# Performance work log

Measured on AMD Instinct MI355X. Metric: run time of the kernel, lower is better.

Reference implementation:

```python
import jax, jax.numpy as jnp
import numpy as np

N_NODES = 50000
N_EDGES = 800000
F_IN = 256
F_OUT = 64
HEADS = 4
LEAKY_ALPHA = 0.2


def setup_inputs() -> dict:
    key = jax.random.key(0)
    ks = jax.random.split(key, 8)
    x = jax.random.normal(ks[0], (N_NODES, F_IN), dtype=jnp.float32)
    W = jax.random.normal(ks[1], (HEADS, F_IN, F_OUT), dtype=jnp.float32) * 0.05
    a_self = jax.random.normal(ks[2], (HEADS, F_OUT), dtype=jnp.float32) * 0.05
    a_neigh = jax.random.normal(ks[3], (HEADS, F_OUT), dtype=jnp.float32) * 0.05
    bias = jnp.zeros((HEADS, F_OUT), dtype=jnp.float32)
    adj_val = jnp.ones((N_EDGES,), dtype=jnp.float32)
    edge_row = jax.random.randint(ks[4], (N_EDGES,), 0, N_NODES, dtype=jnp.int32)
    edge_col = jax.random.randint(ks[5], (N_EDGES,), 0, N_NODES, dtype=jnp.int32)
    return {"x": x, "W": W, "a_self": a_self, "a_neigh": a_neigh,
            "bias": bias, "adj_val": adj_val,
            "edge_row": edge_row, "edge_col": edge_col}


def reference(x, W, a_self, a_neigh, bias, adj_val, edge_row, edge_col):
    N = x.shape[0]
    # per-head projected features: [H, N, F_out]
    feats = jnp.einsum('nf,hfo->hno', x, W)
    # attention logits per node: [H, N]
    s_self = jnp.einsum('hno,ho->hn', feats, a_self)
    s_neigh = jnp.einsum('hno,ho->hn', feats, a_neigh)
    # edge scores at sparse adjacency positions: [H, E]
    z = s_self[:, edge_row] + s_neigh[:, edge_col]
    e = jnp.where(z > 0, z, LEAKY_ALPHA * z) * adj_val[None, :]

    def seg_softmax(e_h):
        # sparse softmax over each row's nonzero entries
        m = jax.ops.segment_max(e_h, edge_row, num_segments=N)
        ex = jnp.exp(e_h - m[edge_row])
        s = jax.ops.segment_sum(ex, edge_row, num_segments=N)
        return ex / s[edge_row]

    alpha = jax.vmap(seg_softmax)(e)  # [H, E]

    def aggregate(alpha_h, feat_h):
        # sparse-dense matmul: out[i] = sum_{j in N(i)} alpha_ij * feat[j]
        return jax.ops.segment_sum(alpha_h[:, None] * feat_h[edge_col],
                                   edge_row, num_segments=N)

    out = jax.vmap(aggregate)(alpha, feats) + bias[:, None, :]  # [H, N, F_out]
    # concat heads -> [N, H*F_out], then activation
    out = jnp.transpose(out, (1, 0, 2)).reshape(N, -1)
    return jax.nn.relu(out)
```

## Files before the change

kernel.cpp:

```cpp
#include <hip/hip_runtime.h>
#include <hip/hip_fp16.h>
#include <math.h>

#define NN 50000
#define NE 800000
#define FIN 256
#define FOUT 64
#define HEADS 4
#define HF 256
#define CAP 64

typedef unsigned short u16;
typedef unsigned int u32;
typedef __attribute__((ext_vector_type(4))) u16 u16x4;
typedef __attribute__((ext_vector_type(8))) u16 u16x8;
typedef __attribute__((ext_vector_type(8))) short short8;
typedef __attribute__((ext_vector_type(4))) float f32x4;

__device__ __forceinline__ u16 f2bf(float x) {
  u32 u = __float_as_uint(x);
  u += 0x7fffu + ((u >> 16) & 1u);
  return (u16)(u >> 16);
}
__device__ __forceinline__ float bf2f(u16 u) {
  return __uint_as_float(((u32)u) << 16);
}
__device__ __forceinline__ void gload_lds16(u16* lds, const u16* g) {
  __builtin_amdgcn_global_load_lds(
      (const __attribute__((address_space(1))) u32*)g,
      (__attribute__((address_space(3))) u32*)lds, 16, 0, 0);
}

#define BT_B   256
#define ZERO_B 196
__global__ __launch_bounds__(256) void tiny_pre_k(const float* __restrict__ W,
                                                  u16* __restrict__ Bt,
                                                  int* __restrict__ cnt) {
  const int b = blockIdx.x, tid = threadIdx.x;
  if (b < BT_B) {
    int t = b * 256 + tid;
    int ho = t >> 8, f = t & 255;
    int h = ho >> 6, o = ho & 63;
    Bt[t] = f2bf(W[h * (FIN * FOUT) + f * FOUT + o]);
  } else {
    int i = (b - BT_B) * 256 + tid;
    if (i < NN) cnt[i] = 0;
  }
}

__global__ __launch_bounds__(512) void gemm_lg_k(const float* __restrict__ X,
                                                 const u16* __restrict__ Bt,
                                                 u16* __restrict__ C,
                                                 const float* __restrict__ a_self,
                                                 const float* __restrict__ a_neigh,
                                                 float* __restrict__ sself,
                                                 float* __restrict__ sneigh,
                                                 int M) {
  __shared__ __align__(16) u16 smA[128 * 64];
  __shared__ __align__(16) u16 smB[256 * 64];
  const int tid = threadIdx.x;
  const int m0 = blockIdx.x * 128;
  const int lane = tid & 63, wid = tid >> 6;
  const int wr = wid >> 2, wc = wid & 3;
  const int arow = tid >> 3;
  const int acol = (tid & 7) * 8;
  f32x4 acc[4][4] = {};

  for (int k0 = 0; k0 < FIN; k0 += 64) {
    float4 p[2][2];
#pragma unroll
    for (int c = 0; c < 2; ++c) {
      int row = m0 + c * 64 + arow;
      if (row > M - 1) row = M - 1;
      const float* ap = X + (size_t)row * 256 + k0 + acol;
      p[c][0] = *(const float4*)ap;
      p[c][1] = *(const float4*)(ap + 4);
    }
#pragma unroll
    for (int c = 0; c < 4; ++c) {
      int row = c * 64 + arow;
      gload_lds16(&smB[(c * 64 + arow) * 64 + acol], Bt + row * 256 + k0 + acol);
    }
#pragma unroll
    for (int c = 0; c < 2; ++c) {
      u16x8 av = { f2bf(p[c][0].x), f2bf(p[c][0].y), f2bf(p[c][0].z), f2bf(p[c][0].w),
                   f2bf(p[c][1].x), f2bf(p[c][1].y), f2bf(p[c][1].z), f2bf(p[c][1].w) };
      *(u16x8*)&smA[(c * 64 + arow) * 64 + acol] = av;
    }
    asm volatile("s_waitcnt vmcnt(0)" ::: "memory");
    __syncthreads();
#pragma unroll
    for (int kk = 0; kk < 2; ++kk) {
      const int kb = kk * 32 + (lane >> 4) * 8;
      short8 aF[4], bF[4];
#pragma unroll
      for (int mi = 0; mi < 4; ++mi)
        aF[mi] = *(const short8*)&smA[(wr * 64 + mi * 16 + (lane & 15)) * 64 + kb];
#pragma unroll
      for (int ni = 0; ni < 4; ++ni)
        bF[ni] = *(const short8*)&smB[(wc * 64 + ni * 16 + (lane & 15)) * 64 + kb];
#pragma unroll
      for (int mi = 0; mi < 4; ++mi)
#pragma unroll
        for (int ni = 0; ni < 4; ++ni)
          acc[mi][ni] = __builtin_amdgcn_mfma_f32_16x16x32_bf16(aF[mi], bF[ni], acc[mi][ni], 0, 0, 0);
    }
    __syncthreads();
  }
#pragma unroll
  for (int mi = 0; mi < 4; ++mi) {
#pragma unroll
    for (int ni = 0; ni < 4; ++ni) {
      f32x4 a = acc[mi][ni];
      int col = wc * 64 + ni * 16 + (lane & 15);
#pragma unroll
      for (int r = 0; r < 4; ++r) {
        int row = m0 + wr * 64 + mi * 16 + (lane >> 4) * 4 + r;
        if (row < M) C[(size_t)row * 256 + col] = f2bf(a[r]);
      }
    }
  }
  float asv[4], anv[4];
#pragma unroll
  for (int ni = 0; ni < 4; ++ni) {
    int col = wc * 64 + ni * 16 + (lane & 15);
    asv[ni] = a_self[col];
    anv[ni] = a_neigh[col];
  }
#pragma unroll
  for (int mi = 0; mi < 4; ++mi) {
#pragma unroll
    for (int r = 0; r < 4; ++r) {
      float ds = 0.f, dn = 0.f;
#pragma unroll
      for (int ni = 0; ni < 4; ++ni) {
        float v = acc[mi][ni][r];
        ds = fmaf(v, asv[ni], ds);
        dn = fmaf(v, anv[ni], dn);
      }
#pragma unroll
      for (int off = 1; off < 16; off <<= 1) {
        ds += __shfl_xor(ds, off, 64);
        dn += __shfl_xor(dn, off, 64);
      }
      if ((lane & 15) == 0) {
        int row = m0 + wr * 64 + mi * 16 + (lane >> 4) * 4 + r;
        if (row < M) {
          sself[row * 4 + wc] = ds;
          sneigh[row * 4 + wc] = dn;
        }
      }
    }
  }
}

__global__ __launch_bounds__(256) void scatter_wk(const int* __restrict__ erow,
                                                  const int* __restrict__ ecol,
                                                  const float* __restrict__ adj,
                                                  const float4* __restrict__ sself4,
                                                  const float4* __restrict__ sneigh4,
                                                  int* __restrict__ cnt,
                                                  u16* __restrict__ scol,
                                                  u16x4* __restrict__ swt) {
  int e = blockIdx.x * 256 + threadIdx.x;
  int r = erow[e];
  int c = ecol[e];
  float av = adj[e];
  float4 ss = sself4[r];
  float4 nb = sneigh4[c];
  float z0 = ss.x + nb.x, z1 = ss.y + nb.y, z2 = ss.z + nb.z, z3 = ss.w + nb.w;
  float w0 = __expf((z0 > 0.f ? z0 : 0.2f * z0) * av);
  float w1 = __expf((z1 > 0.f ? z1 : 0.2f * z1) * av);
  float w2 = __expf((z2 > 0.f ? z2 : 0.2f * z2) * av);
  float w3 = __expf((z3 > 0.f ? z3 : 0.2f * z3) * av);
  __half2 h01 = __floats2half2_rn(w0, w1);
  __half2 h23 = __floats2half2_rn(w2, w3);
  u32 u01 = *(u32*)&h01, u23 = *(u32*)&h23;
  int p = atomicAdd(&cnt[r], 1);
  if (p < CAP) {
    int slot = r * CAP + p;
    scol[slot] = (u16)c;
    u16x4 wv = { (u16)(u01 & 0xffff), (u16)(u01 >> 16),
                 (u16)(u23 & 0xffff), (u16)(u23 >> 16) };
    swt[slot] = wv;
  }
}

#define NODE_B 2048
__global__ __launch_bounds__(256) void node5_k(const int* __restrict__ cnt,
                                               const u16* __restrict__ scol,
                                               const u16x4* __restrict__ swt,
                                               const u16* __restrict__ fb,
                                               const float* __restrict__ bias,
                                               float* __restrict__ out) {
  const int tid = threadIdx.x;
  const int l = tid & 31;
  const int hsel = l >> 4;
  const int hw0 = blockIdx.x * 8 + (tid >> 5);
  const float4 b0 = ((const float4*)bias)[l];
  const float4 b1 = ((const float4*)bias)[32 + l];

  for (int i = hw0; i < NN; i += NODE_B * 8) {
    const int deg = min(cnt[i], CAP);
    const int beg = i * CAP;
    float s0 = 0.f, s1 = 0.f;
    float4 acc0 = { 0.f, 0.f, 0.f, 0.f };
    float4 acc1 = { 0.f, 0.f, 0.f, 0.f };

    for (int base = 0; base < deg; base += 32) {
      const int cnt32 = min(32, deg - base);
      const int idx = beg + base + min(l, cnt32 - 1);
      int colv = (int)scol[idx];
      u16x4 wv4 = swt[idx];
      u32 wy = ((u32)wv4[0]) | ((u32)wv4[1] << 16);
      u32 wz = ((u32)wv4[2]) | ((u32)wv4[3] << 16);
      if (l >= cnt32) { wy = 0u; wz = 0u; }
      const int c8 = (cnt32 + 7) & ~7;
      for (int e = 0; e < c8; e += 8) {
        int colq[8]; float wa[8], wb[8];
#pragma unroll
        for (int q = 0; q < 8; ++q) {
          colq[q] = __shfl(colv, e + q, 32);
          u32 y = (u32)__shfl((int)wy, e + q, 32);
          u32 z = (u32)__shfl((int)wz, e + q, 32);
          float2 fy = __half22float2(*(const __half2*)&y);
          float2 fz = __half22float2(*(const __half2*)&z);
          wa[q] = hsel ? fy.y : fy.x;
          wb[q] = hsel ? fz.y : fz.x;
        }
        u16x4 f0[8], f1[8];
#pragma unroll
        for (int q = 0; q < 8; ++q) {
          const u16* fp = fb + (size_t)colq[q] * HF + l * 4;
          f0[q] = *(const u16x4*)fp;
          f1[q] = *(const u16x4*)(fp + 128);
        }
#pragma unroll
        for (int q = 0; q < 8; ++q) {
          s0 += wa[q];
          s1 += wb[q];
          acc0.x = fmaf(wa[q], bf2f(f0[q][0]), acc0.x);
          acc0.y = fmaf(wa[q], bf2f(f0[q][1]), acc0.y);
          acc0.z = fmaf(wa[q], bf2f(f0[q][2]), acc0.z);
          acc0.w = fmaf(wa[q], bf2f(f0[q][3]), acc0.w);
          acc1.x = fmaf(wb[q], bf2f(f1[q][0]), acc1.x);
          acc1.y = fmaf(wb[q], bf2f(f1[q][1]), acc1.y);
          acc1.z = fmaf(wb[q], bf2f(f1[q][2]), acc1.z);
          acc1.w = fmaf(wb[q], bf2f(f1[q][3]), acc1.w);
        }
      }
    }
    const float rs0 = (s0 > 0.f) ? __frcp_rn(s0) : 0.f;
    const float rs1 = (s1 > 0.f) ? __frcp_rn(s1) : 0.f;
    float4 o0, o1;
    o0.x = fmaxf(fmaf(acc0.x, rs0, b0.x), 0.f);
    o0.y = fmaxf(fmaf(acc0.y, rs0, b0.y), 0.f);
    o0.z = fmaxf(fmaf(acc0.z, rs0, b0.z), 0.f);
    o0.w = fmaxf(fmaf(acc0.w, rs0, b0.w), 0.f);
    o1.x = fmaxf(fmaf(acc1.x, rs1, b1.x), 0.f);
    o1.y = fmaxf(fmaf(acc1.y, rs1, b1.y), 0.f);
    o1.z = fmaxf(fmaf(acc1.z, rs1, b1.z), 0.f);
    o1.w = fmaxf(fmaf(acc1.w, rs1, b1.w), 0.f);
    ((float4*)out)[(size_t)i * 64 + l] = o0;
    ((float4*)out)[(size_t)i * 64 + 32 + l] = o1;
  }
}

extern "C" void kernel_launch(void* const* d_in, const int* in_sizes, int n_in,
                              void* d_out, int out_size, void* d_ws, size_t ws_size,
                              hipStream_t stream) {
  const float* x       = (const float*)d_in[0];
  const float* W       = (const float*)d_in[1];
  const float* a_self  = (const float*)d_in[2];
  const float* a_neigh = (const float*)d_in[3];
  const float* bias    = (const float*)d_in[4];
  const float* adj     = (const float*)d_in[5];
  const int*   erow    = (const int*)d_in[6];
  const int*   ecol    = (const int*)d_in[7];
  float* out = (float*)d_out;

  char* w = (char*)d_ws;
  u16*   Bt     = (u16*)w;   w += 131072;
  u16*   fb     = (u16*)w;   w += 25600000;
  float* sself  = (float*)w; w += 800000;
  float* sneigh = (float*)w; w += 800000;
  int*   cnt    = (int*)w;   w += 200064;
  u16*   scol   = (u16*)w;  w += NN * CAP * 2;
  u16x4* swt    = (u16x4*)w; w += NN * CAP * 8;

  tiny_pre_k<<<dim3(BT_B + ZERO_B), dim3(256), 0, stream>>>(W, Bt, cnt);
  gemm_lg_k<<<dim3((NN + 127) / 128), dim3(512), 0, stream>>>(x, Bt, fb, a_self, a_neigh,
                                                              sself, sneigh, NN);
  scatter_wk<<<dim3(NE / 256), dim3(256), 0, stream>>>(erow, ecol, adj,
                                                       (const float4*)sself,
                                                       (const float4*)sneigh,
                                                       cnt, scol, swt);
  node5_k<<<dim3(NODE_B), dim3(256), 0, stream>>>(cnt, scol, swt, fb, bias, out);
}
```

Measured before the change: 142.1 us.

## Move edge-weight computation into node kernel and pack col/adj into one slot

New measurement: 147.1 us. 1.04x slower.

```diff
diff --git a/kernel.cpp b/kernel.cpp
--- a/kernel.cpp
+++ b/kernel.cpp
@@ -46,6 +46,21 @@
     int i = (b - BT_B) * 256 + tid;
     if (i < NN) cnt[i] = 0;
   }
+}
+
+__global__ __launch_bounds__(256) void scatter_k(const int* __restrict__ erow,
+                                                 const int* __restrict__ ecol,
+                                                 const float* __restrict__ adj,
+                                                 int* __restrict__ cnt,
+                                                 u32* __restrict__ slots) {
+  int e = blockIdx.x * 256 + threadIdx.x;
+  int r = erow[e];
+  int c = ecol[e];
+  float av = adj[e];
+  __half ha = __float2half_rn(av);
+  u32 rec = (u32)c | ((u32)(*(u16*)&ha) << 16);
+  int p = atomicAdd(&cnt[r], 1);
+  if (p < CAP) slots[r * CAP + p] = rec;
 }
 
 __global__ __launch_bounds__(512) void gemm_lg_k(const float* __restrict__ X,
@@ -154,42 +169,11 @@
   }
 }
 
-__global__ __launch_bounds__(256) void scatter_wk(const int* __restrict__ erow,
-                                                  const int* __restrict__ ecol,
-                                                  const float* __restrict__ adj,
-                                                  const float4* __restrict__ sself4,
-                                                  const float4* __restrict__ sneigh4,
-                                                  int* __restrict__ cnt,
-                                                  u16* __restrict__ scol,
-                                                  u16x4* __restrict__ swt) {
-  int e = blockIdx.x * 256 + threadIdx.x;
-  int r = erow[e];
-  int c = ecol[e];
-  float av = adj[e];
-  float4 ss = sself4[r];
-  float4 nb = sneigh4[c];
-  float z0 = ss.x + nb.x, z1 = ss.y + nb.y, z2 = ss.z + nb.z, z3 = ss.w + nb.w;
-  float w0 = __expf((z0 > 0.f ? z0 : 0.2f * z0) * av);
-  float w1 = __expf((z1 > 0.f ? z1 : 0.2f * z1) * av);
-  float w2 = __expf((z2 > 0.f ? z2 : 0.2f * z2) * av);
-  float w3 = __expf((z3 > 0.f ? z3 : 0.2f * z3) * av);
-  __half2 h01 = __floats2half2_rn(w0, w1);
-  __half2 h23 = __floats2half2_rn(w2, w3);
-  u32 u01 = *(u32*)&h01, u23 = *(u32*)&h23;
-  int p = atomicAdd(&cnt[r], 1);
-  if (p < CAP) {
-    int slot = r * CAP + p;
-    scol[slot] = (u16)c;
-    u16x4 wv = { (u16)(u01 & 0xffff), (u16)(u01 >> 16),
-                 (u16)(u23 & 0xffff), (u16)(u23 >> 16) };
-    swt[slot] = wv;
-  }
-}
-
 #define NODE_B 2048
-__global__ __launch_bounds__(256) void node5_k(const int* __restrict__ cnt,
-                                               const u16* __restrict__ scol,
-                                               const u16x4* __restrict__ swt,
+__global__ __launch_bounds__(256) void node6_k(const int* __restrict__ cnt,
+                                               const u32* __restrict__ slots,
+                                               const float4* __restrict__ sself4,
+                                               const float4* __restrict__ sneigh4,
                                                const u16* __restrict__ fb,
                                                const float* __restrict__ bias,
                                                float* __restrict__ out) {
@@ -203,19 +187,30 @@
   for (int i = hw0; i < NN; i += NODE_B * 8) {
     const int deg = min(cnt[i], CAP);
     const int beg = i * CAP;
+    const float4 ssv = sself4[i];
     float s0 = 0.f, s1 = 0.f;
     float4 acc0 = { 0.f, 0.f, 0.f, 0.f };
     float4 acc1 = { 0.f, 0.f, 0.f, 0.f };
 
     for (int base = 0; base < deg; base += 32) {
-      const int cnt32 = min(32, deg - base);
-      const int idx = beg + base + min(l, cnt32 - 1);
-      int colv = (int)scol[idx];
-      u16x4 wv4 = swt[idx];
-      u32 wy = ((u32)wv4[0]) | ((u32)wv4[1] << 16);
-      u32 wz = ((u32)wv4[2]) | ((u32)wv4[3] << 16);
-      if (l >= cnt32) { wy = 0u; wz = 0u; }
-      const int c8 = (cnt32 + 7) & ~7;
+      const int c32 = min(32, deg - base);
+      u32 sv = slots[beg + base + min(l, c32 - 1)];
+      int colv = (int)(sv & 0xFFFFu);
+      u16 ah = (u16)(sv >> 16);
+      float av = __half2float(*(const __half*)&ah);
+      float4 nb = sneigh4[colv];
+      float z0 = ssv.x + nb.x, z1 = ssv.y + nb.y;
+      float z2 = ssv.z + nb.z, z3 = ssv.w + nb.w;
+      float w0 = __expf((z0 > 0.f ? z0 : 0.2f * z0) * av);
+      float w1 = __expf((z1 > 0.f ? z1 : 0.2f * z1) * av);
+      float w2 = __expf((z2 > 0.f ? z2 : 0.2f * z2) * av);
+      float w3 = __expf((z3 > 0.f ? z3 : 0.2f * z3) * av);
+      if (l >= c32) { w0 = 0.f; w1 = 0.f; w2 = 0.f; w3 = 0.f; }
+      __half2 h01 = __floats2half2_rn(w0, w1);
+      __half2 h23 = __floats2half2_rn(w2, w3);
+      u32 wy = *(u32*)&h01, wz = *(u32*)&h23;
+
+      const int c8 = (c32 + 7) & ~7;
       for (int e = 0; e < c8; e += 8) {
         int colq[8]; float wa[8], wb[8];
 #pragma unroll
@@ -285,15 +280,14 @@
   float* sself  = (float*)w; w += 800000;
   float* sneigh = (float*)w; w += 800000;
   int*   cnt    = (int*)w;   w += 200064;
-  u16*   scol   = (u16*)w;  w += NN * CAP * 2;
-  u16x4* swt    = (u16x4*)w; w += NN * CAP * 8;
+  u32*   slots  = (u32*)w;   w += NN * CAP * 4;
 
   tiny_pre_k<<<dim3(BT_B + ZERO_B), dim3(256), 0, stream>>>(W, Bt, cnt);
+  scatter_k<<<dim3(NE / 256), dim3(256), 0, stream>>>(erow, ecol, adj, cnt, slots);
   gemm_lg_k<<<dim3((NN + 127) / 128), dim3(512), 0, stream>>>(x, Bt, fb, a_self, a_neigh,
                                                               sself, sneigh, NN);
-  scatter_wk<<<dim3(NE / 256), dim3(256), 0, stream>>>(erow, ecol, adj,
-                                                       (const float4*)sself,
-                                                       (const float4*)sneigh,
-                                                       cnt, scol, swt);
-  node5_k<<<dim3(NODE_B), dim3(256), 0, stream>>>(cnt, scol, swt, fb, bias, out);
-}
+  node6_k<<<dim3(NODE_B), dim3(256), 0, stream>>>(cnt, slots,
+                                                  (const float4*)sself,
+                                                  (const float4*)sneigh,
+                                                  fb, bias, out);
+}
```
